# Optimization experiments

Measured on AMD Instinct MI355X. Metric: run time of the kernel, lower is better.

The kernel has to match this reference:

```python
import jax, jax.numpy as jnp
import numpy as np

NX = 768
N_HEAD = 12
N_CTX = 2048
BATCH = 4
EPS = 1e-5
NEG = -1000000000.0


def _layernorm(x, g, b):
    # NOTE: faithful to source bug: returns g + normalized + b (additive, not scale)
    u = jnp.mean(x, axis=-1, keepdims=True)
    s = jnp.mean((x - u) ** 2, axis=-1, keepdims=True)
    return g + (x - u) / jnp.sqrt(s + EPS) + b


def setup_inputs() -> dict:
    key = jax.random.key(0)
    ks = jax.random.split(key, 8)
    std = 0.02
    x = jax.random.normal(ks[0], (BATCH, N_CTX, NX), dtype=jnp.float32)
    w_attn = jax.random.normal(ks[1], (NX, 3 * NX), dtype=jnp.float32) * std
    b_attn = jnp.zeros((3 * NX,), jnp.float32)
    w_proj = jax.random.normal(ks[2], (NX, NX), dtype=jnp.float32) * std
    b_proj = jnp.zeros((NX,), jnp.float32)
    ln1_g = jnp.ones((NX,), jnp.float32)
    ln1_b = jnp.zeros((NX,), jnp.float32)
    w_fc = jax.random.normal(ks[3], (NX, 4 * NX), dtype=jnp.float32) * std
    b_fc = jnp.zeros((4 * NX,), jnp.float32)
    w_fc2 = jax.random.normal(ks[4], (4 * NX, NX), dtype=jnp.float32) * std
    b_fc2 = jnp.zeros((NX,), jnp.float32)
    ln2_g = jnp.ones((NX,), jnp.float32)
    ln2_b = jnp.zeros((NX,), jnp.float32)
    return dict(x=x, w_attn=w_attn, b_attn=b_attn, w_proj=w_proj, b_proj=b_proj,
                ln1_g=ln1_g, ln1_b=ln1_b, w_fc=w_fc, b_fc=b_fc,
                w_fc2=w_fc2, b_fc2=b_fc2, ln2_g=ln2_g, ln2_b=ln2_b)


def reference(x, w_attn, b_attn, w_proj, b_proj, ln1_g, ln1_b,
              w_fc, b_fc, w_fc2, b_fc2, ln2_g, ln2_b):
    B, S, D = x.shape
    dh = D // N_HEAD
    # --- attention (scale=False: no 1/sqrt(d)) ---
    qkv = x @ w_attn + b_attn                      # [B,S,3D]
    q, k, v = jnp.split(qkv, 3, axis=-1)
    q = q.reshape(B, S, N_HEAD, dh).transpose(0, 2, 1, 3)   # [B,H,S,dh]
    k = k.reshape(B, S, N_HEAD, dh).transpose(0, 2, 3, 1)   # [B,H,dh,S]
    v = v.reshape(B, S, N_HEAD, dh).transpose(0, 2, 1, 3)   # [B,H,S,dh]
    w = jnp.einsum('bhsd,bhdt->bhst', q, k)        # [B,H,S,S]
    mask = jnp.tril(jnp.ones((S, S), x.dtype))[None, None]
    w = w * mask + NEG * (1.0 - mask)
    w = jax.nn.softmax(w, axis=-1)
    a = jnp.einsum('bhst,bhtd->bhsd', w, v)        # [B,H,S,dh]
    a = a.transpose(0, 2, 1, 3).reshape(B, S, D)
    a = a @ w_proj + b_proj
    # dropout layers are identity (eval mode)
    n = _layernorm(x + a, ln1_g, ln1_b)
    # --- MLP (intended ReLU; source's nn.ReLU usage is a bug) ---
    h = jax.nn.relu(n @ w_fc + b_fc)
    m = h @ w_fc2 + b_fc2
    return _layernorm(n + m, ln2_g, ln2_b)
```

## Files before the change

### kernel.cpp

```cpp
#include <hip/hip_runtime.h>
#include <stdint.h>

#define NX 768
#define SEQ 2048
#define NHEAD 12
#define MROWS 8192
#define LN_EPS 1e-5f
#define MASK_NEG -1000000000.0f

typedef __bf16 bf16x8 __attribute__((ext_vector_type(8)));
typedef float f32x4 __attribute__((ext_vector_type(4)));

#define AS3(p)  ((__attribute__((address_space(3))) void*)(p))
#define AS1C(p) ((const __attribute__((address_space(1))) void*)(p))

__device__ __forceinline__ unsigned short f2bf(float f) {
  union { float f; unsigned int u; } v; v.f = f;
  unsigned int r = v.u + 0x7fffu + ((v.u >> 16) & 1u);
  return (unsigned short)(r >> 16);
}
__device__ __forceinline__ float bf2f(unsigned short u) {
  union { unsigned int u; float f; } v; v.u = ((unsigned int)u) << 16;
  return v.f;
}

__global__ void convert_f32_bf16(const float* __restrict__ in,
                                 unsigned short* __restrict__ out, int n4) {
  int i = blockIdx.x * blockDim.x + threadIdx.x;
  if (i >= n4) return;
  float4 v = ((const float4*)in)[i];
  ushort4 o;
  o.x = f2bf(v.x); o.y = f2bf(v.y); o.z = f2bf(v.z); o.w = f2bf(v.w);
  ((ushort4*)out)[i] = o;
}

__global__ void transpose_w(const float* __restrict__ w,
                            unsigned short* __restrict__ wt, int K, int N) {
  __shared__ float tile[32][33];
  int n0 = blockIdx.x * 32, k0 = blockIdx.y * 32;
  int tx = threadIdx.x, ty = threadIdx.y;
#pragma unroll
  for (int j = 0; j < 4; ++j)
    tile[ty + j * 8][tx] = w[(long)(k0 + ty + j * 8) * N + n0 + tx];
  __syncthreads();
#pragma unroll
  for (int j = 0; j < 4; ++j)
    wt[(long)(n0 + ty + j * 8) * K + k0 + tx] = f2bf(tile[tx][ty + j * 8]);
}

__global__ void transpose_v(const unsigned short* __restrict__ qkv,
                            unsigned short* __restrict__ vt) {
  __shared__ unsigned short tile[64][68];
  int s0 = blockIdx.x * 64;
  int bh = blockIdx.y, b = bh / NHEAD, h = bh % NHEAD;
  int tx = threadIdx.x, ty = threadIdx.y;
  const unsigned short* src = qkv + (long)b * SEQ * 2304 + 1536 + h * 64;
#pragma unroll
  for (int j = 0; j < 4; ++j) {
    int s = ty + j * 16;
    ushort4 vv = *(const ushort4*)(src + (long)(s0 + s) * 2304 + tx * 4);
    *(ushort4*)(&tile[s][tx * 4]) = vv;
  }
  __syncthreads();
  unsigned short* dst = vt + (long)bh * 64 * SEQ + s0;
#pragma unroll
  for (int j = 0; j < 4; ++j) {
    int d = ty + j * 16;
    ushort4 o;
    o.x = tile[tx * 4 + 0][d]; o.y = tile[tx * 4 + 1][d];
    o.z = tile[tx * 4 + 2][d]; o.w = tile[tx * 4 + 3][d];
    *(ushort4*)(dst + (long)d * SEQ + tx * 4) = o;
  }
}

template <int ACT, int BN>
__global__ __launch_bounds__(256) void gemm_bt(const unsigned short* __restrict__ A,
                                               const unsigned short* __restrict__ Bt,
                                               const float* __restrict__ bias,
                                               unsigned short* __restrict__ C,
                                               int Nsz, int K) {
  constexpr int ABUF = 128 * 64;
  constexpr int BBUF = BN * 64;
  constexpr int BUF = ABUF + BBUF;
  __shared__ __align__(16) unsigned short smem[2 * BUF];
  const int tid = threadIdx.x;
  const int w = tid >> 6, lane = tid & 63;
  const int l15 = lane & 15, quad = lane >> 4;
  constexpr int MT = (BN == 128) ? 4 : 2;
  const int wrow0 = (BN == 128) ? (w >> 1) * 64 : w * 32;
  const int wcol0 = (BN == 128) ? (w & 1) * 64 : 0;
  const long m0 = (long)blockIdx.x * 128;
  const long n0 = (long)blockIdx.y * BN;

  const int srow = tid >> 3;
  const int sg = tid & 7;

  const unsigned short* ap[4];
#pragma unroll
  for (int p = 0; p < 4; ++p) {
    int row = p * 32 + srow;
    ap[p] = A + (m0 + row) * (long)K + (sg ^ (row & 7)) * 8;
  }
  const unsigned short* bp[BN / 32];
#pragma unroll
  for (int p = 0; p < BN / 32; ++p) {
    int row = p * 32 + srow;
    bp[p] = Bt + (n0 + row) * (long)K + (sg ^ (row & 7)) * 8;
  }

  auto stage = [&](int kb) {
    unsigned short* As = smem + (kb & 1) * BUF;
    unsigned short* Bs = As + ABUF;
#pragma unroll
    for (int p = 0; p < 4; ++p) {
      __builtin_amdgcn_global_load_lds(AS1C(ap[p]), AS3(As + p * 2048 + w * 512), 16, 0, 0);
      ap[p] += 64;
    }
#pragma unroll
    for (int p = 0; p < BN / 32; ++p) {
      __builtin_amdgcn_global_load_lds(AS1C(bp[p]), AS3(Bs + p * 2048 + w * 512), 16, 0, 0);
      bp[p] += 64;
    }
  };

  f32x4 acc[MT][4] = {};
  const int nkb = K / 64;

  stage(0);
  for (int kb = 0; kb < nkb; ++kb) {
    __syncthreads();
    if (kb + 1 < nkb) stage(kb + 1);
    const unsigned short* As = smem + (kb & 1) * BUF;
    const unsigned short* Bs = As + ABUF;
#pragma unroll
    for (int s2 = 0; s2 < 2; ++s2) {
      const int phys = ((s2 * 4 + quad) ^ (l15 & 7)) * 8;
      bf16x8 af[MT], bfr[4];
#pragma unroll
      for (int mt = 0; mt < MT; ++mt)
        af[mt] = *(const bf16x8*)(As + (wrow0 + mt * 16 + l15) * 64 + phys);
#pragma unroll
      for (int nt = 0; nt < 4; ++nt)
        bfr[nt] = *(const bf16x8*)(Bs + (wcol0 + nt * 16 + l15) * 64 + phys);
#pragma unroll
      for (int mt = 0; mt < MT; ++mt)
#pragma unroll
        for (int nt = 0; nt < 4; ++nt)
          acc[mt][nt] = __builtin_amdgcn_mfma_f32_16x16x32_bf16(af[mt], bfr[nt], acc[mt][nt], 0, 0, 0);
    }
  }
  __syncthreads();

  unsigned short* Ew = smem + w * (16 * 72);
  const long gmB = m0 + wrow0;
  const long gnB = n0 + wcol0;
  float bv[4];
#pragma unroll
  for (int nt = 0; nt < 4; ++nt) bv[nt] = bias[gnB + nt * 16 + l15];
  const int prow = lane >> 3, pcol = (lane & 7) * 8;
#pragma unroll
  for (int mt = 0; mt < MT; ++mt) {
#pragma unroll
    for (int nt = 0; nt < 4; ++nt)
#pragma unroll
      for (int r = 0; r < 4; ++r) {
        float v = acc[mt][nt][r] + bv[nt];
        if (ACT == 1) v = fmaxf(v, 0.f);
        Ew[(quad * 4 + r) * 72 + nt * 16 + l15] = f2bf(v);
      }
#pragma unroll
    for (int ps = 0; ps < 2; ++ps) {
      int row = ps * 8 + prow;
      int4 t = *(const int4*)(Ew + row * 72 + pcol);
      *(int4*)(C + (gmB + mt * 16 + row) * (long)Nsz + gnB + pcol) = t;
    }
  }
}

__global__ __launch_bounds__(256) void attn_v9(const unsigned short* __restrict__ qkv,
                                               const unsigned short* __restrict__ vt,
                                               unsigned short* __restrict__ out) {
  const int blk = blockIdx.x;
  const int bh_lo = blk & 7;
  const int j = blk >> 3;
  const int bx = j & 15;
  const int bh = (j >> 4) * 8 + bh_lo;
  const int b = bh / NHEAD, h = bh % NHEAD;
  const int tid = threadIdx.x;
  const int w = tid >> 6, lane = tid & 63, l15 = lane & 15, quad = lane >> 4;

  __shared__ __align__(16) unsigned short Ks[2][64 * 64];
  __shared__ __align__(16) unsigned short Vs[2][64 * 64];
  __shared__ __align__(16) unsigned short Ps[4][16 * 64];

  const long rowbase = (long)b * SEQ;
  unsigned short* Pw = &Ps[w][0];
  const unsigned short* vbh = vt + (long)bh * 64 * SEQ;
  const float LOG2E = 1.4426950408889634f;

  const int krow = tid >> 3;
  const int kgo = (((tid & 7) ^ (krow & 7)) * 8);
  const unsigned short* kbase = qkv + rowbase * 2304L + 768 + h * 64;

  for (int pass = 0; pass < 2; ++pass) {
    const int qt = (pass == 0) ? bx : 31 - bx;
    const int niter = qt + 1;
    const int qrow = qt * 64 + w * 16 + l15;
    const int qg = qrow;

    bf16x8 qf[2];
#pragma unroll
    for (int s2 = 0; s2 < 2; ++s2) {
      int4 raw = *(const int4*)(qkv + (rowbase + qrow) * 2304L + h * 64 + s2 * 32 + quad * 8);
      const unsigned short* rp = (const unsigned short*)&raw;
#pragma unroll
      for (int j2 = 0; j2 < 8; ++j2)
        qf[s2][j2] = (__bf16)(bf2f(rp[j2]) * LOG2E);
    }

    const unsigned short* kp[2];
    const unsigned short* vp[2];
#pragma unroll
    for (int p = 0; p < 2; ++p) {
      kp[p] = kbase + (long)(p * 32 + krow) * 2304 + kgo;
      vp[p] = vbh + (long)(p * 32 + krow) * SEQ + kgo;
    }

    float l_sum = 0.f;
    f32x4 o_acc[4] = {};

    __syncthreads();
#pragma unroll
    for (int p = 0; p < 2; ++p) {
      __builtin_amdgcn_global_load_lds(AS1C(kp[p]), AS3(&Ks[0][0] + p * 2048 + w * 512), 16, 0, 0);
      __builtin_amdgcn_global_load_lds(AS1C(vp[p]), AS3(&Vs[0][0] + p * 2048 + w * 512), 16, 0, 0);
      kp[p] += 64 * 2304;
      vp[p] += 64;
    }

    for (int it = 0; it < niter; ++it) {
      __syncthreads();
      if (it + 1 < niter) {
        const int nb = (it + 1) & 1;
#pragma unroll
        for (int p = 0; p < 2; ++p) {
          __builtin_amdgcn_global_load_lds(AS1C(kp[p]), AS3(&Ks[nb][0] + p * 2048 + w * 512), 16, 0, 0);
          __builtin_amdgcn_global_load_lds(AS1C(vp[p]), AS3(&Vs[nb][0] + p * 2048 + w * 512), 16, 0, 0);
          kp[p] += 64 * 2304;
          vp[p] += 64;
        }
      }
      const unsigned short* Kc = &Ks[it & 1][0];
      const unsigned short* Vc = &Vs[it & 1][0];

      f32x4 st[4] = {};
      __builtin_amdgcn_s_setprio(1);
#pragma unroll
      for (int nt = 0; nt < 4; ++nt) {
        int key = nt * 16 + l15;
#pragma unroll
        for (int s2 = 0; s2 < 2; ++s2) {
          int phys = (s2 * 4 + quad) ^ (key & 7);
          bf16x8 kf = *(const bf16x8*)(Kc + key * 64 + phys * 8);
          st[nt] = __builtin_amdgcn_mfma_f32_16x16x32_bf16(kf, qf[s2], st[nt], 0, 0, 0);
        }
      }
      __builtin_amdgcn_s_setprio(0);

      if (it == niter - 1) {
#pragma unroll
        for (int nt = 0; nt < 4; ++nt) {
          int kg = it * 64 + nt * 16 + quad * 4;
#pragma unroll
          for (int r = 0; r < 4; ++r)
            if (kg + r > qg) st[nt][r] = MASK_NEG;
        }
      }

      float sn[4];
#pragma unroll
      for (int nt = 0; nt < 4; ++nt) {
        float p0 = __builtin_amdgcn_exp2f(st[nt][0]);
        float p1 = __builtin_amdgcn_exp2f(st[nt][1]);
        float p2 = __builtin_amdgcn_exp2f(st[nt][2]);
        float p3 = __builtin_amdgcn_exp2f(st[nt][3]);
        st[nt][0] = p0; st[nt][1] = p1; st[nt][2] = p2; st[nt][3] = p3;
        sn[nt] = (p0 + p1) + (p2 + p3);
      }
      l_sum += (sn[0] + sn[1]) + (sn[2] + sn[3]);

#pragma unroll
      for (int nt = 0; nt < 4; ++nt) {
        unsigned int lo, hi;
        asm("v_cvt_pk_bf16_f32 %0, %1, %2" : "=v"(lo) : "v"(st[nt][0]), "v"(st[nt][1]));
        asm("v_cvt_pk_bf16_f32 %0, %1, %2" : "=v"(hi) : "v"(st[nt][2]), "v"(st[nt][3]));
        int g8 = (nt * 2 + (quad >> 1)) ^ (l15 & 7);
        uint2 pv; pv.x = lo; pv.y = hi;
        *(uint2*)(Pw + l15 * 64 + g8 * 8 + (quad & 1) * 4) = pv;
      }

      __builtin_amdgcn_s_setprio(1);
#pragma unroll
      for (int c = 0; c < 2; ++c) {
        int phys = ((c * 4 + quad) ^ (l15 & 7)) * 8;
        bf16x8 pf = *(const bf16x8*)(Pw + l15 * 64 + phys);
#pragma unroll
        for (int ntd = 0; ntd < 4; ++ntd) {
          int d = ntd * 16 + l15;
          bf16x8 vf = *(const bf16x8*)(Vc + d * 64 + phys);
          o_acc[ntd] = __builtin_amdgcn_mfma_f32_16x16x32_bf16(pf, vf, o_acc[ntd], 0, 0, 0);
        }
      }
      __builtin_amdgcn_s_setprio(0);
    }

    l_sum += __shfl_xor(l_sum, 16);
    l_sum += __shfl_xor(l_sum, 32);
#pragma unroll
    for (int r = 0; r < 4; ++r) {
      float lq = __shfl(l_sum, quad * 4 + r);
      float inv = 1.f / lq;
      int q = qt * 64 + w * 16 + quad * 4 + r;
#pragma unroll
      for (int ntd = 0; ntd < 4; ++ntd) {
        int d = ntd * 16 + l15;
        out[(rowbase + q) * (long)NX + h * 64 + d] = f2bf(o_acc[ntd][r] * inv);
      }
    }
  }
}

__global__ __launch_bounds__(256) void add_ln(const float* __restrict__ x_f,
                                              const unsigned short* __restrict__ x_b,
                                              const unsigned short* __restrict__ y_b,
                                              const float* __restrict__ g,
                                              const float* __restrict__ beta,
                                              float* __restrict__ out_f,
                                              unsigned short* __restrict__ out_b) {
  const int row = blockIdx.x, t = threadIdx.x;
  const long base = (long)row * NX;
  float v[3];
#pragma unroll
  for (int j = 0; j < 3; ++j) {
    int i = t + j * 256;
    float a = x_f ? x_f[base + i] : bf2f(x_b[base + i]);
    v[j] = a + bf2f(y_b[base + i]);
  }
  __shared__ float red[4];
  int wv = t >> 6, ln = t & 63;

  float ssum = v[0] + v[1] + v[2];
#pragma unroll
  for (int sh = 32; sh >= 1; sh >>= 1) ssum += __shfl_xor(ssum, sh);
  if (ln == 0) red[wv] = ssum;
  __syncthreads();
  float u = (red[0] + red[1] + red[2] + red[3]) * (1.f / NX);
  __syncthreads();

  float d0 = v[0] - u, d1 = v[1] - u, d2 = v[2] - u;
  float sq = d0 * d0 + d1 * d1 + d2 * d2;
#pragma unroll
  for (int sh = 32; sh >= 1; sh >>= 1) sq += __shfl_xor(sq, sh);
  if (ln == 0) red[wv] = sq;
  __syncthreads();
  float s = (red[0] + red[1] + red[2] + red[3]) * (1.f / NX);
  float rinv = rsqrtf(s + LN_EPS);

  float dd[3] = {d0, d1, d2};
#pragma unroll
  for (int j = 0; j < 3; ++j) {
    int i = t + j * 256;
    float o = g[i] + dd[j] * rinv + beta[i];
    if (out_f) out_f[base + i] = o;
    else out_b[base + i] = f2bf(o);
  }
}

extern "C" void kernel_launch(void* const* d_in, const int* in_sizes, int n_in,
                              void* d_out, int out_size, void* d_ws, size_t ws_size,
                              hipStream_t stream) {
  const float* x      = (const float*)d_in[0];
  const float* w_attn = (const float*)d_in[1];
  const float* b_attn = (const float*)d_in[2];
  const float* w_proj = (const float*)d_in[3];
  const float* b_proj = (const float*)d_in[4];
  const float* ln1_g  = (const float*)d_in[5];
  const float* ln1_b  = (const float*)d_in[6];
  const float* w_fc   = (const float*)d_in[7];
  const float* b_fc   = (const float*)d_in[8];
  const float* w_fc2  = (const float*)d_in[9];
  const float* b_fc2  = (const float*)d_in[10];
  const float* ln2_g  = (const float*)d_in[11];
  const float* ln2_b  = (const float*)d_in[12];
  float* out = (float*)d_out;

  char* ws = (char*)d_ws;
  size_t off = 0;
  auto alloc = [&](size_t bytes) {
    char* p = ws + off;
    off += (bytes + 255) & ~(size_t)255;
    return p;
  };
  unsigned short* xb      = (unsigned short*)alloc((size_t)MROWS * NX * 2);
  unsigned short* wt_attn = (unsigned short*)alloc((size_t)2304 * 768 * 2);
  unsigned short* wt_proj = (unsigned short*)alloc((size_t)768 * 768 * 2);
  unsigned short* wt_fc   = (unsigned short*)alloc((size_t)3072 * 768 * 2);
  unsigned short* wt_fc2  = (unsigned short*)alloc((size_t)768 * 3072 * 2);
  unsigned short* qkv     = (unsigned short*)alloc((size_t)MROWS * 3072 * 2);
  unsigned short* hbuf    = qkv;
  unsigned short* abuf    = (unsigned short*)alloc((size_t)MROWS * NX * 2);
  unsigned short* mbuf    = abuf;
  unsigned short* nbuf    = (unsigned short*)alloc((size_t)MROWS * NX * 2);
  unsigned short* vtb     = nbuf;
  unsigned short* pout    = xb;

  convert_f32_bf16<<<(MROWS * NX / 4 + 255) / 256, 256, 0, stream>>>(x, xb, MROWS * NX / 4);
  transpose_w<<<dim3(2304 / 32, 768 / 32), dim3(32, 8), 0, stream>>>(w_attn, wt_attn, 768, 2304);
  transpose_w<<<dim3(768 / 32, 768 / 32), dim3(32, 8), 0, stream>>>(w_proj, wt_proj, 768, 768);
  transpose_w<<<dim3(3072 / 32, 768 / 32), dim3(32, 8), 0, stream>>>(w_fc, wt_fc, 768, 3072);
  transpose_w<<<dim3(768 / 32, 3072 / 32), dim3(32, 8), 0, stream>>>(w_fc2, wt_fc2, 3072, 768);

  gemm_bt<0, 64><<<dim3(MROWS / 128, 2304 / 64), 256, 0, stream>>>(xb, wt_attn, b_attn, qkv, 2304, 768);
  transpose_v<<<dim3(SEQ / 64, 48), dim3(16, 16), 0, stream>>>(qkv, vtb);
  attn_v9<<<768, 256, 0, stream>>>(qkv, vtb, abuf);
  gemm_bt<0, 64><<<dim3(MROWS / 128, 768 / 64), 256, 0, stream>>>(abuf, wt_proj, b_proj, pout, 768, 768);
  add_ln<<<MROWS, 256, 0, stream>>>(x, nullptr, pout, ln1_g, ln1_b, nullptr, nbuf);
  gemm_bt<1, 128><<<dim3(MROWS / 128, 3072 / 128), 256, 0, stream>>>(nbuf, wt_fc, b_fc, hbuf, 3072, 768);
  gemm_bt<0, 64><<<dim3(MROWS / 128, 768 / 64), 256, 0, stream>>>(hbuf, wt_fc2, b_fc2, mbuf, 768, 3072);
  add_ln<<<MROWS, 256, 0, stream>>>(nullptr, nbuf, mbuf, ln2_g, ln2_b, out, nullptr);
}
```

Before: 339.8 us.

## Fuse paired causal query tiles into one K/V sweep in attention

```diff
diff --git a/kernel.cpp b/kernel.cpp
--- a/kernel.cpp
+++ b/kernel.cpp
@@ -13,6 +13,8 @@
 
 #define AS3(p)  ((__attribute__((address_space(3))) void*)(p))
 #define AS1C(p) ((const __attribute__((address_space(1))) void*)(p))
+
+template <bool B> struct BoolC { static constexpr bool value = B; };
 
 __device__ __forceinline__ unsigned short f2bf(float f) {
   union { float f; unsigned int u; } v; v.f = f;
@@ -177,24 +179,29 @@
   }
 }
 
-__global__ __launch_bounds__(256) void attn_v9(const unsigned short* __restrict__ qkv,
-                                               const unsigned short* __restrict__ vt,
-                                               unsigned short* __restrict__ out) {
+__global__ __launch_bounds__(256) void attn_v10(const unsigned short* __restrict__ qkv,
+                                                const unsigned short* __restrict__ vt,
+                                                unsigned short* __restrict__ out) {
   const int blk = blockIdx.x;
   const int bh_lo = blk & 7;
   const int j = blk >> 3;
-  const int bx = j & 15;
-  const int bh = (j >> 4) * 8 + bh_lo;
+  const int bx = j / 6;
+  const int bh = (j % 6) * 8 + bh_lo;
   const int b = bh / NHEAD, h = bh % NHEAD;
   const int tid = threadIdx.x;
   const int w = tid >> 6, lane = tid & 63, l15 = lane & 15, quad = lane >> 4;
 
+  const int qtA = 31 - bx;
+  const int qtB = bx;
+  const int niter = qtA + 1;
+
   __shared__ __align__(16) unsigned short Ks[2][64 * 64];
   __shared__ __align__(16) unsigned short Vs[2][64 * 64];
-  __shared__ __align__(16) unsigned short Ps[4][16 * 64];
+  __shared__ __align__(16) unsigned short Ps[4][2 * 16 * 64];
 
   const long rowbase = (long)b * SEQ;
-  unsigned short* Pw = &Ps[w][0];
+  unsigned short* PwA = &Ps[w][0];
+  unsigned short* PwB = PwA + 16 * 64;
   const unsigned short* vbh = vt + (long)bh * 64 * SEQ;
   const float LOG2E = 1.4426950408889634f;
 
@@ -202,118 +209,138 @@
   const int kgo = (((tid & 7) ^ (krow & 7)) * 8);
   const unsigned short* kbase = qkv + rowbase * 2304L + 768 + h * 64;
 
-  for (int pass = 0; pass < 2; ++pass) {
-    const int qt = (pass == 0) ? bx : 31 - bx;
-    const int niter = qt + 1;
-    const int qrow = qt * 64 + w * 16 + l15;
-    const int qg = qrow;
-
-    bf16x8 qf[2];
-#pragma unroll
-    for (int s2 = 0; s2 < 2; ++s2) {
-      int4 raw = *(const int4*)(qkv + (rowbase + qrow) * 2304L + h * 64 + s2 * 32 + quad * 8);
-      const unsigned short* rp = (const unsigned short*)&raw;
-#pragma unroll
-      for (int j2 = 0; j2 < 8; ++j2)
-        qf[s2][j2] = (__bf16)(bf2f(rp[j2]) * LOG2E);
-    }
-
-    const unsigned short* kp[2];
-    const unsigned short* vp[2];
-#pragma unroll
-    for (int p = 0; p < 2; ++p) {
-      kp[p] = kbase + (long)(p * 32 + krow) * 2304 + kgo;
-      vp[p] = vbh + (long)(p * 32 + krow) * SEQ + kgo;
-    }
-
-    float l_sum = 0.f;
-    f32x4 o_acc[4] = {};
-
+  const int qrowA = qtA * 64 + w * 16 + l15;
+  const int qrowB = qtB * 64 + w * 16 + l15;
+  const int qgA = qrowA, qgB = qrowB;
+  bf16x8 qfA[2], qfB[2];
+#pragma unroll
+  for (int s2 = 0; s2 < 2; ++s2) {
+    int4 rawA = *(const int4*)(qkv + (rowbase + qrowA) * 2304L + h * 64 + s2 * 32 + quad * 8);
+    int4 rawB = *(const int4*)(qkv + (rowbase + qrowB) * 2304L + h * 64 + s2 * 32 + quad * 8);
+    const unsigned short* rpA = (const unsigned short*)&rawA;
+    const unsigned short* rpB = (const unsigned short*)&rawB;
+#pragma unroll
+    for (int j2 = 0; j2 < 8; ++j2) {
+      qfA[s2][j2] = (__bf16)(bf2f(rpA[j2]) * LOG2E);
+      qfB[s2][j2] = (__bf16)(bf2f(rpB[j2]) * LOG2E);
+    }
+  }
+
+  const unsigned short* kp[2];
+  const unsigned short* vp[2];
+#pragma unroll
+  for (int p = 0; p < 2; ++p) {
+    kp[p] = kbase + (long)(p * 32 + krow) * 2304 + kgo;
+    vp[p] = vbh + (long)(p * 32 + krow) * SEQ + kgo;
+  }
+
+  float l_sumA = 0.f, l_sumB = 0.f;
+  f32x4 o_accA[4] = {}, o_accB[4] = {};
+
+#pragma unroll
+  for (int p = 0; p < 2; ++p) {
+    __builtin_amdgcn_global_load_lds(AS1C(kp[p]), AS3(&Ks[0][0] + p * 2048 + w * 512), 16, 0, 0);
+    __builtin_amdgcn_global_load_lds(AS1C(vp[p]), AS3(&Vs[0][0] + p * 2048 + w * 512), 16, 0, 0);
+    kp[p] += 64 * 2304;
+    vp[p] += 64;
+  }
+
+  auto smpack = [&](f32x4* st, unsigned short* Pslab, float& lsum) {
+    float sn[4];
+#pragma unroll
+    for (int nt = 0; nt < 4; ++nt) {
+      float p0 = __builtin_amdgcn_exp2f(st[nt][0]);
+      float p1 = __builtin_amdgcn_exp2f(st[nt][1]);
+      float p2 = __builtin_amdgcn_exp2f(st[nt][2]);
+      float p3 = __builtin_amdgcn_exp2f(st[nt][3]);
+      sn[nt] = (p0 + p1) + (p2 + p3);
+      unsigned int lo, hi;
+      asm("v_cvt_pk_bf16_f32 %0, %1, %2" : "=v"(lo) : "v"(p0), "v"(p1));
+      asm("v_cvt_pk_bf16_f32 %0, %1, %2" : "=v"(hi) : "v"(p2), "v"(p3));
+      int g8 = (nt * 2 + (quad >> 1)) ^ (l15 & 7);
+      uint2 pv; pv.x = lo; pv.y = hi;
+      *(uint2*)(Pslab + l15 * 64 + g8 * 8 + (quad & 1) * 4) = pv;
+    }
+    lsum += (sn[0] + sn[1]) + (sn[2] + sn[3]);
+  };
+
+  auto body = [&](const unsigned short* Kc, const unsigned short* Vc, int it, auto DOB) {
+    constexpr bool doB = decltype(DOB)::value;
+    f32x4 stA[4] = {}, stB[4] = {};
+
+    __builtin_amdgcn_s_setprio(1);
+#pragma unroll
+    for (int nt = 0; nt < 4; ++nt) {
+      int key = nt * 16 + l15;
+#pragma unroll
+      for (int s2 = 0; s2 < 2; ++s2) {
+        int phys = (s2 * 4 + quad) ^ (key & 7);
+        bf16x8 kf = *(const bf16x8*)(Kc + key * 64 + phys * 8);
+        stA[nt] = __builtin_amdgcn_mfma_f32_16x16x32_bf16(kf, qfA[s2], stA[nt], 0, 0, 0);
+        if (doB) stB[nt] = __builtin_amdgcn_mfma_f32_16x16x32_bf16(kf, qfB[s2], stB[nt], 0, 0, 0);
+      }
+    }
+    __builtin_amdgcn_s_setprio(0);
+
+    if (it == qtA) {
+#pragma unroll
+      for (int nt = 0; nt < 4; ++nt) {
+        int kg = it * 64 + nt * 16 + quad * 4;
+#pragma unroll
+        for (int r = 0; r < 4; ++r)
+          if (kg + r > qgA) stA[nt][r] = MASK_NEG;
+      }
+    }
+    if (doB && it == qtB) {
+#pragma unroll
+      for (int nt = 0; nt < 4; ++nt) {
+        int kg = it * 64 + nt * 16 + quad * 4;
+#pragma unroll
+        for (int r = 0; r < 4; ++r)
+          if (kg + r > qgB) stB[nt][r] = MASK_NEG;
+      }
+    }
+
+    smpack(stA, PwA, l_sumA);
+    if (doB) smpack(stB, PwB, l_sumB);
+
+    __builtin_amdgcn_s_setprio(1);
+#pragma unroll
+    for (int c = 0; c < 2; ++c) {
+      int phys = ((c * 4 + quad) ^ (l15 & 7)) * 8;
+      bf16x8 pfA = *(const bf16x8*)(PwA + l15 * 64 + phys);
+      bf16x8 pfB;
+      if (doB) pfB = *(const bf16x8*)(PwB + l15 * 64 + phys);
+#pragma unroll
+      for (int ntd = 0; ntd < 4; ++ntd) {
+        int d = ntd * 16 + l15;
+        bf16x8 vf = *(const bf16x8*)(Vc + d * 64 + phys);
+        o_accA[ntd] = __builtin_amdgcn_mfma_f32_16x16x32_bf16(pfA, vf, o_accA[ntd], 0, 0, 0);
+        if (doB) o_accB[ntd] = __builtin_amdgcn_mfma_f32_16x16x32_bf16(pfB, vf, o_accB[ntd], 0, 0, 0);
+      }
+    }
+    __builtin_amdgcn_s_setprio(0);
+  };
+
+  for (int it = 0; it < niter; ++it) {
     __syncthreads();
-#pragma unroll
-    for (int p = 0; p < 2; ++p) {
-      __builtin_amdgcn_global_load_lds(AS1C(kp[p]), AS3(&Ks[0][0] + p * 2048 + w * 512), 16, 0, 0);
-      __builtin_amdgcn_global_load_lds(AS1C(vp[p]), AS3(&Vs[0][0] + p * 2048 + w * 512), 16, 0, 0);
-      kp[p] += 64 * 2304;
-      vp[p] += 64;
-    }
-
-    for (int it = 0; it < niter; ++it) {
-      __syncthreads();
-      if (it + 1 < niter) {
-        const int nb = (it + 1) & 1;
-#pragma unroll
-        for (int p = 0; p < 2; ++p) {
-          __builtin_amdgcn_global_load_lds(AS1C(kp[p]), AS3(&Ks[nb][0] + p * 2048 + w * 512), 16, 0, 0);
-          __builtin_amdgcn_global_load_lds(AS1C(vp[p]), AS3(&Vs[nb][0] + p * 2048 + w * 512), 16, 0, 0);
-          kp[p] += 64 * 2304;
-          vp[p] += 64;
-        }
-      }
-      const unsigned short* Kc = &Ks[it & 1][0];
-      const unsigned short* Vc = &Vs[it & 1][0];
-
-      f32x4 st[4] = {};
-      __builtin_amdgcn_s_setprio(1);
-#pragma unroll
-      for (int nt = 0; nt < 4; ++nt) {
-        int key = nt * 16 + l15;
-#pragma unroll
-        for (int s2 = 0; s2 < 2; ++s2) {
-          int phys = (s2 * 4 + quad) ^ (key & 7);
-          bf16x8 kf = *(const bf16x8*)(Kc + key * 64 + phys * 8);
-          st[nt] = __builtin_amdgcn_mfma_f32_16x16x32_bf16(kf, qf[s2], st[nt], 0, 0, 0);
-        }
-      }
-      __builtin_amdgcn_s_setprio(0);
-
-      if (it == niter - 1) {
-#pragma unroll
-        for (int nt = 0; nt < 4; ++nt) {
-          int kg = it * 64 + nt * 16 + quad * 4;
-#pragma unroll
-          for (int r = 0; r < 4; ++r)
-            if (kg + r > qg) st[nt][r] = MASK_NEG;
-        }
-      }
-
-      float sn[4];
-#pragma unroll
-      for (int nt = 0; nt < 4; ++nt) {
-        float p0 = __builtin_amdgcn_exp2f(st[nt][0]);
-        float p1 = __builtin_amdgcn_exp2f(st[nt][1]);
-        float p2 = __builtin_amdgcn_exp2f(st[nt][2]);
-        float p3 = __builtin_amdgcn_exp2f(st[nt][3]);
-        st[nt][0] = p0; st[nt][1] = p1; st[nt][2] = p2; st[nt][3] = p3;
-        sn[nt] = (p0 + p1) + (p2 + p3);
-      }
-      l_sum += (sn[0] + sn[1]) + (sn[2] + sn[3]);
-
-#pragma unroll
-      for (int nt = 0; nt < 4; ++nt) {
-        unsigned int lo, hi;
-        asm("v_cvt_pk_bf16_f32 %0, %1, %2" : "=v"(lo) : "v"(st[nt][0]), "v"(st[nt][1]));
-        asm("v_cvt_pk_bf16_f32 %0, %1, %2" : "=v"(hi) : "v"(st[nt][2]), "v"(st[nt][3]));
-        int g8 = (nt * 2 + (quad >> 1)) ^ (l15 & 7);
-        uint2 pv; pv.x = lo; pv.y = hi;
-        *(uint2*)(Pw + l15 * 64 + g8 * 8 + (quad & 1) * 4) = pv;
-      }
-
-      __builtin_amdgcn_s_setprio(1);
-#pragma unroll
-      for (int c = 0; c < 2; ++c) {
-        int phys = ((c * 4 + quad) ^ (l15 & 7)) * 8;
-        bf16x8 pf = *(const bf16x8*)(Pw + l15 * 64 + phys);
-#pragma unroll
-        for (int ntd = 0; ntd < 4; ++ntd) {
-          int d = ntd * 16 + l15;
-          bf16x8 vf = *(const bf16x8*)(Vc + d * 64 + phys);
-          o_acc[ntd] = __builtin_amdgcn_mfma_f32_16x16x32_bf16(pf, vf, o_acc[ntd], 0, 0, 0);
-        }
-      }
-      __builtin_amdgcn_s_setprio(0);
-    }
-
+    if (it + 1 < niter) {
+      const int nb = (it + 1) & 1;
+#pragma unroll
+      for (int p = 0; p < 2; ++p) {
+        __builtin_amdgcn_global_load_lds(AS1C(kp[p]), AS3(&Ks[nb][0] + p * 2048 + w * 512), 16, 0, 0);
+        __builtin_amdgcn_global_load_lds(AS1C(vp[p]), AS3(&Vs[nb][0] + p * 2048 + w * 512), 16, 0, 0);
+        kp[p] += 64 * 2304;
+        vp[p] += 64;
+      }
+    }
+    const unsigned short* Kc = &Ks[it & 1][0];
+    const unsigned short* Vc = &Vs[it & 1][0];
+    if (it <= qtB) body(Kc, Vc, it, BoolC<true>{});
+    else           body(Kc, Vc, it, BoolC<false>{});
+  }
+
+  auto epi = [&](float l_sum, f32x4* o_acc, int qt) {
     l_sum += __shfl_xor(l_sum, 16);
     l_sum += __shfl_xor(l_sum, 32);
 #pragma unroll
@@ -327,7 +354,9 @@
         out[(rowbase + q) * (long)NX + h * 64 + d] = f2bf(o_acc[ntd][r] * inv);
       }
     }
-  }
+  };
+  epi(l_sumA, o_accA, qtA);
+  epi(l_sumB, o_accB, qtB);
 }
 
 __global__ __launch_bounds__(256) void add_ln(const float* __restrict__ x_f,
@@ -422,7 +451,7 @@
 
   gemm_bt<0, 64><<<dim3(MROWS / 128, 2304 / 64), 256, 0, stream>>>(xb, wt_attn, b_attn, qkv, 2304, 768);
   transpose_v<<<dim3(SEQ / 64, 48), dim3(16, 16), 0, stream>>>(qkv, vtb);
-  attn_v9<<<768, 256, 0, stream>>>(qkv, vtb, abuf);
+  attn_v10<<<768, 256, 0, stream>>>(qkv, vtb, abuf);
   gemm_bt<0, 64><<<dim3(MROWS / 128, 768 / 64), 256, 0, stream>>>(abuf, wt_proj, b_proj, pout, 768, 768);
   add_ln<<<MROWS, 256, 0, stream>>>(x, nullptr, pout, ln1_g, ln1_b, nullptr, nbuf);
   gemm_bt<1, 128><<<dim3(MROWS / 128, 3072 / 128), 256, 0, stream>>>(nbuf, wt_fc, b_fc, hbuf, 3072, 768);
```

New measurement: 357.2 us. 5.1% more time.

## Process both causal query tiles concurrently with 8 waves sharing K/V loads

Applied to the files above, without the earlier changes.

```diff
diff --git a/kernel.cpp b/kernel.cpp
--- a/kernel.cpp
+++ b/kernel.cpp
@@ -177,9 +177,9 @@
   }
 }
 
-__global__ __launch_bounds__(256) void attn_v9(const unsigned short* __restrict__ qkv,
-                                               const unsigned short* __restrict__ vt,
-                                               unsigned short* __restrict__ out) {
+__global__ __launch_bounds__(512) void attn_v11(const unsigned short* __restrict__ qkv,
+                                                const unsigned short* __restrict__ vt,
+                                                unsigned short* __restrict__ out) {
   const int blk = blockIdx.x;
   const int bh_lo = blk & 7;
   const int j = blk >> 3;
@@ -187,11 +187,20 @@
   const int bh = (j >> 4) * 8 + bh_lo;
   const int b = bh / NHEAD, h = bh % NHEAD;
   const int tid = threadIdx.x;
-  const int w = tid >> 6, lane = tid & 63, l15 = lane & 15, quad = lane >> 4;
+  const int w = tid >> 6;
+  const int wl = w & 3;
+  const int g = w >> 2;
+  const int lane = tid & 63, l15 = lane & 15, quad = lane >> 4;
+
+  const int qtA = 31 - bx;
+  const int qtB = bx;
+  const int qt = g ? qtB : qtA;
+  const int niter = qtA + 1;
+  const int nact = qt + 1;
 
   __shared__ __align__(16) unsigned short Ks[2][64 * 64];
   __shared__ __align__(16) unsigned short Vs[2][64 * 64];
-  __shared__ __align__(16) unsigned short Ps[4][16 * 64];
+  __shared__ __align__(16) unsigned short Ps[8][16 * 64];
 
   const long rowbase = (long)b * SEQ;
   unsigned short* Pw = &Ps[w][0];
@@ -201,131 +210,114 @@
   const int krow = tid >> 3;
   const int kgo = (((tid & 7) ^ (krow & 7)) * 8);
   const unsigned short* kbase = qkv + rowbase * 2304L + 768 + h * 64;
-
-  for (int pass = 0; pass < 2; ++pass) {
-    const int qt = (pass == 0) ? bx : 31 - bx;
-    const int niter = qt + 1;
-    const int qrow = qt * 64 + w * 16 + l15;
-    const int qg = qrow;
-
-    bf16x8 qf[2];
-#pragma unroll
-    for (int s2 = 0; s2 < 2; ++s2) {
-      int4 raw = *(const int4*)(qkv + (rowbase + qrow) * 2304L + h * 64 + s2 * 32 + quad * 8);
-      const unsigned short* rp = (const unsigned short*)&raw;
-#pragma unroll
-      for (int j2 = 0; j2 < 8; ++j2)
-        qf[s2][j2] = (__bf16)(bf2f(rp[j2]) * LOG2E);
-    }
-
-    const unsigned short* kp[2];
-    const unsigned short* vp[2];
-#pragma unroll
-    for (int p = 0; p < 2; ++p) {
-      kp[p] = kbase + (long)(p * 32 + krow) * 2304 + kgo;
-      vp[p] = vbh + (long)(p * 32 + krow) * SEQ + kgo;
-    }
-
-    float l_sum = 0.f;
-    f32x4 o_acc[4] = {};
-
+  const unsigned short* kp = kbase + (long)krow * 2304 + kgo;
+  const unsigned short* vp = vbh + (long)krow * SEQ + kgo;
+
+  const int qrow = qt * 64 + wl * 16 + l15;
+  const int qg = qrow;
+  bf16x8 qf[2];
+#pragma unroll
+  for (int s2 = 0; s2 < 2; ++s2) {
+    int4 raw = *(const int4*)(qkv + (rowbase + qrow) * 2304L + h * 64 + s2 * 32 + quad * 8);
+    const unsigned short* rp = (const unsigned short*)&raw;
+#pragma unroll
+    for (int j2 = 0; j2 < 8; ++j2)
+      qf[s2][j2] = (__bf16)(bf2f(rp[j2]) * LOG2E);
+  }
+
+  float l_sum = 0.f;
+  f32x4 o_acc[4] = {};
+
+  __builtin_amdgcn_global_load_lds(AS1C(kp), AS3(&Ks[0][0] + w * 512), 16, 0, 0);
+  __builtin_amdgcn_global_load_lds(AS1C(vp), AS3(&Vs[0][0] + w * 512), 16, 0, 0);
+  kp += 64 * 2304;
+  vp += 64;
+
+  for (int it = 0; it < niter; ++it) {
     __syncthreads();
-#pragma unroll
-    for (int p = 0; p < 2; ++p) {
-      __builtin_amdgcn_global_load_lds(AS1C(kp[p]), AS3(&Ks[0][0] + p * 2048 + w * 512), 16, 0, 0);
-      __builtin_amdgcn_global_load_lds(AS1C(vp[p]), AS3(&Vs[0][0] + p * 2048 + w * 512), 16, 0, 0);
-      kp[p] += 64 * 2304;
-      vp[p] += 64;
-    }
-
-    for (int it = 0; it < niter; ++it) {
-      __syncthreads();
-      if (it + 1 < niter) {
-        const int nb = (it + 1) & 1;
-#pragma unroll
-        for (int p = 0; p < 2; ++p) {
-          __builtin_amdgcn_global_load_lds(AS1C(kp[p]), AS3(&Ks[nb][0] + p * 2048 + w * 512), 16, 0, 0);
-          __builtin_amdgcn_global_load_lds(AS1C(vp[p]), AS3(&Vs[nb][0] + p * 2048 + w * 512), 16, 0, 0);
-          kp[p] += 64 * 2304;
-          vp[p] += 64;
-        }
+    if (it + 1 < niter) {
+      const int nb = (it + 1) & 1;
+      __builtin_amdgcn_global_load_lds(AS1C(kp), AS3(&Ks[nb][0] + w * 512), 16, 0, 0);
+      __builtin_amdgcn_global_load_lds(AS1C(vp), AS3(&Vs[nb][0] + w * 512), 16, 0, 0);
+      kp += 64 * 2304;
+      vp += 64;
+    }
+    if (it >= nact) continue;
+    const unsigned short* Kc = &Ks[it & 1][0];
+    const unsigned short* Vc = &Vs[it & 1][0];
+
+    f32x4 st[4] = {};
+    __builtin_amdgcn_s_setprio(1);
+#pragma unroll
+    for (int nt = 0; nt < 4; ++nt) {
+      int key = nt * 16 + l15;
+#pragma unroll
+      for (int s2 = 0; s2 < 2; ++s2) {
+        int phys = (s2 * 4 + quad) ^ (key & 7);
+        bf16x8 kf = *(const bf16x8*)(Kc + key * 64 + phys * 8);
+        st[nt] = __builtin_amdgcn_mfma_f32_16x16x32_bf16(kf, qf[s2], st[nt], 0, 0, 0);
       }
-      const unsigned short* Kc = &Ks[it & 1][0];
-      const unsigned short* Vc = &Vs[it & 1][0];
-
-      f32x4 st[4] = {};
-      __builtin_amdgcn_s_setprio(1);
+    }
+    __builtin_amdgcn_s_setprio(0);
+
+    if (it == qt) {
 #pragma unroll
       for (int nt = 0; nt < 4; ++nt) {
-        int key = nt * 16 + l15;
-#pragma unroll
-        for (int s2 = 0; s2 < 2; ++s2) {
-          int phys = (s2 * 4 + quad) ^ (key & 7);
-          bf16x8 kf = *(const bf16x8*)(Kc + key * 64 + phys * 8);
-          st[nt] = __builtin_amdgcn_mfma_f32_16x16x32_bf16(kf, qf[s2], st[nt], 0, 0, 0);
-        }
+        int kg = it * 64 + nt * 16 + quad * 4;
+#pragma unroll
+        for (int r = 0; r < 4; ++r)
+          if (kg + r > qg) st[nt][r] = MASK_NEG;
       }
-      __builtin_amdgcn_s_setprio(0);
-
-      if (it == niter - 1) {
-#pragma unroll
-        for (int nt = 0; nt < 4; ++nt) {
-          int kg = it * 64 + nt * 16 + quad * 4;
-#pragma unroll
-          for (int r = 0; r < 4; ++r)
-            if (kg + r > qg) st[nt][r] = MASK_NEG;
-        }
-      }
-
-      float sn[4];
-#pragma unroll
-      for (int nt = 0; nt < 4; ++nt) {
-        float p0 = __builtin_amdgcn_exp2f(st[nt][0]);
-        float p1 = __builtin_amdgcn_exp2f(st[nt][1]);
-        float p2 = __builtin_amdgcn_exp2f(st[nt][2]);
-        float p3 = __builtin_amdgcn_exp2f(st[nt][3]);
-        st[nt][0] = p0; st[nt][1] = p1; st[nt][2] = p2; st[nt][3] = p3;
-        sn[nt] = (p0 + p1) + (p2 + p3);
-      }
-      l_sum += (sn[0] + sn[1]) + (sn[2] + sn[3]);
-
-#pragma unroll
-      for (int nt = 0; nt < 4; ++nt) {
-        unsigned int lo, hi;
-        asm("v_cvt_pk_bf16_f32 %0, %1, %2" : "=v"(lo) : "v"(st[nt][0]), "v"(st[nt][1]));
-        asm("v_cvt_pk_bf16_f32 %0, %1, %2" : "=v"(hi) : "v"(st[nt][2]), "v"(st[nt][3]));
-        int g8 = (nt * 2 + (quad >> 1)) ^ (l15 & 7);
-        uint2 pv; pv.x = lo; pv.y = hi;
-        *(uint2*)(Pw + l15 * 64 + g8 * 8 + (quad & 1) * 4) = pv;
-      }
-
-      __builtin_amdgcn_s_setprio(1);
-#pragma unroll
-      for (int c = 0; c < 2; ++c) {
-        int phys = ((c * 4 + quad) ^ (l15 & 7)) * 8;
-        bf16x8 pf = *(const bf16x8*)(Pw + l15 * 64 + phys);
-#pragma unroll
-        for (int ntd = 0; ntd < 4; ++ntd) {
-          int d = ntd * 16 + l15;
-          bf16x8 vf = *(const bf16x8*)(Vc + d * 64 + phys);
-          o_acc[ntd] = __builtin_amdgcn_mfma_f32_16x16x32_bf16(pf, vf, o_acc[ntd], 0, 0, 0);
-        }
-      }
-      __builtin_amdgcn_s_setprio(0);
-    }
-
-    l_sum += __shfl_xor(l_sum, 16);
-    l_sum += __shfl_xor(l_sum, 32);
-#pragma unroll
-    for (int r = 0; r < 4; ++r) {
-      float lq = __shfl(l_sum, quad * 4 + r);
-      float inv = 1.f / lq;
-      int q = qt * 64 + w * 16 + quad * 4 + r;
+    }
+
+    float sn[4];
+#pragma unroll
+    for (int nt = 0; nt < 4; ++nt) {
+      float p0 = __builtin_amdgcn_exp2f(st[nt][0]);
+      float p1 = __builtin_amdgcn_exp2f(st[nt][1]);
+      float p2 = __builtin_amdgcn_exp2f(st[nt][2]);
+      float p3 = __builtin_amdgcn_exp2f(st[nt][3]);
+      st[nt][0] = p0; st[nt][1] = p1; st[nt][2] = p2; st[nt][3] = p3;
+      sn[nt] = (p0 + p1) + (p2 + p3);
+    }
+    l_sum += (sn[0] + sn[1]) + (sn[2] + sn[3]);
+
+#pragma unroll
+    for (int nt = 0; nt < 4; ++nt) {
+      unsigned int lo, hi;
+      asm("v_cvt_pk_bf16_f32 %0, %1, %2" : "=v"(lo) : "v"(st[nt][0]), "v"(st[nt][1]));
+      asm("v_cvt_pk_bf16_f32 %0, %1, %2" : "=v"(hi) : "v"(st[nt][2]), "v"(st[nt][3]));
+      int g8 = (nt * 2 + (quad >> 1)) ^ (l15 & 7);
+      uint2 pv; pv.x = lo; pv.y = hi;
+      *(uint2*)(Pw + l15 * 64 + g8 * 8 + (quad & 1) * 4) = pv;
+    }
+
+    __builtin_amdgcn_s_setprio(1);
+#pragma unroll
+    for (int c = 0; c < 2; ++c) {
+      int phys = ((c * 4 + quad) ^ (l15 & 7)) * 8;
+      bf16x8 pf = *(const bf16x8*)(Pw + l15 * 64 + phys);
 #pragma unroll
       for (int ntd = 0; ntd < 4; ++ntd) {
         int d = ntd * 16 + l15;
-        out[(rowbase + q) * (long)NX + h * 64 + d] = f2bf(o_acc[ntd][r] * inv);
+        bf16x8 vf = *(const bf16x8*)(Vc + d * 64 + phys);
+        o_acc[ntd] = __builtin_amdgcn_mfma_f32_16x16x32_bf16(pf, vf, o_acc[ntd], 0, 0, 0);
       }
+    }
+    __builtin_amdgcn_s_setprio(0);
+  }
+
+  l_sum += __shfl_xor(l_sum, 16);
+  l_sum += __shfl_xor(l_sum, 32);
+#pragma unroll
+  for (int r = 0; r < 4; ++r) {
+    float lq = __shfl(l_sum, quad * 4 + r);
+    float inv = 1.f / lq;
+    int q = qt * 64 + wl * 16 + quad * 4 + r;
+#pragma unroll
+    for (int ntd = 0; ntd < 4; ++ntd) {
+      int d = ntd * 16 + l15;
+      out[(rowbase + q) * (long)NX + h * 64 + d] = f2bf(o_acc[ntd][r] * inv);
     }
   }
 }
@@ -422,7 +414,7 @@
 
   gemm_bt<0, 64><<<dim3(MROWS / 128, 2304 / 64), 256, 0, stream>>>(xb, wt_attn, b_attn, qkv, 2304, 768);
   transpose_v<<<dim3(SEQ / 64, 48), dim3(16, 16), 0, stream>>>(qkv, vtb);
-  attn_v9<<<768, 256, 0, stream>>>(qkv, vtb, abuf);
+  attn_v11<<<768, 512, 0, stream>>>(qkv, vtb, abuf);
   gemm_bt<0, 64><<<dim3(MROWS / 128, 768 / 64), 256, 0, stream>>>(abuf, wt_proj, b_proj, pout, 768, 768);
   add_ln<<<MROWS, 256, 0, stream>>>(x, nullptr, pout, ln1_g, ln1_b, nullptr, nbuf);
   gemm_bt<1, 128><<<dim3(MROWS / 128, 3072 / 128), 256, 0, stream>>>(nbuf, wt_fc, b_fc, hbuf, 3072, 768);
```

Measured after the change: 343.1 us. About the same (+1.0%).
